# Optimization experiments

Measured on AMD Instinct MI355X. Metric: run time of the kernel, lower is better.

Reference implementation:

```python
import jax, jax.numpy as jnp
import numpy as np


def setup_inputs() -> dict:
    key = jax.random.key(0)
    k1, k2, k3 = jax.random.split(key, 3)
    B, C, H, W = 64, 512, 32, 32
    l = jax.random.normal(k1, (B, C, H, W), dtype=jnp.float32)
    g = jax.random.normal(k2, (B, C), dtype=jnp.float32)
    # 1x1 Conv2d(C -> 1, bias=False) weight, flattened from [1, C, 1, 1] to [C]
    w = jax.random.normal(k3, (C,), dtype=jnp.float32) * (1.0 / np.sqrt(C))
    return {"l": l, "g": g, "w": w}


def reference(l, g, w):
    B, C, H, W = l.shape
    # broadcast add of global vector, then 1x1 conv == channel dot-product
    x = l + g[:, :, None, None]                      # [B, C, H, W]
    c = jnp.einsum('bchw,c->bhw', x, w)              # [B, H, W]
    # softmax over the flattened spatial dims
    a = jax.nn.softmax(c.reshape(B, -1), axis=1).reshape(B, 1, H, W)
    # attention-weighted spatial pooling of l -> [B, C]
    g_out = jnp.einsum('bchw,bzhw->bc', l, a)
    return (c[:, None, :, :], g_out)
```

## Files before the change

### kernel.cpp

```cpp
#include <hip/hip_runtime.h>

#define B_  64
#define C_  512
#define HW_ 1024
#define NCHUNK 16
#define CPC (C_ / NCHUNK)

__device__ __forceinline__ float waveReduceSum(float v) {
    #pragma unroll
    for (int off = 32; off > 0; off >>= 1) v += __shfl_xor(v, off);
    return v;
}

__device__ __forceinline__ float waveReduceMax(float v) {
    #pragma unroll
    for (int off = 32; off > 0; off >>= 1) v = fmaxf(v, __shfl_xor(v, off));
    return v;
}

__global__ __launch_bounds__(256) void k1_partial_dot(
        const float* __restrict__ l,
        const float* __restrict__ w,
        float* __restrict__ part) {
    const int blk   = blockIdx.x;
    const int b     = blk / NCHUNK;
    const int chunk = blk % NCHUNK;
    const int tid   = threadIdx.x;

    const float4* l4 = reinterpret_cast<const float4*>(
        l + ((size_t)b * C_ + (size_t)chunk * CPC) * HW_);

    float4 acc = {0.f, 0.f, 0.f, 0.f};
    #pragma unroll 8
    for (int i = 0; i < CPC; ++i) {
        const float wv = w[chunk * CPC + i];
        const float4 v = l4[(size_t)i * (HW_ / 4) + tid];
        acc.x = fmaf(v.x, wv, acc.x);
        acc.y = fmaf(v.y, wv, acc.y);
        acc.z = fmaf(v.z, wv, acc.z);
        acc.w = fmaf(v.w, wv, acc.w);
    }
    reinterpret_cast<float4*>(part)[(size_t)blk * (HW_ / 4) + tid] = acc;
}

__global__ __launch_bounds__(1024) void k2_softmax(
        const float* __restrict__ part,
        const float* __restrict__ g,
        const float* __restrict__ w,
        float* __restrict__ c_out,
        float* __restrict__ a_out) {
    __shared__ float lds[16];
    const int b   = blockIdx.x;
    const int tid = threadIdx.x;
    const int lane = tid & 63;
    const int wid  = tid >> 6;

    float p = (tid < C_) ? g[b * C_ + tid] * w[tid] : 0.f;
    p = waveReduceSum(p);
    if (lane == 0) lds[wid] = p;
    __syncthreads();
    if (wid == 0) {
        float x = (lane < 16) ? lds[lane] : 0.f;
        x = waveReduceSum(x);
        if (lane == 0) lds[0] = x;
    }
    __syncthreads();
    const float gw = lds[0];
    __syncthreads();

    float cv = gw;
    #pragma unroll
    for (int k = 0; k < NCHUNK; ++k)
        cv += part[((size_t)b * NCHUNK + k) * HW_ + tid];

    float m = waveReduceMax(cv);
    if (lane == 0) lds[wid] = m;
    __syncthreads();
    if (wid == 0) {
        float x = (lane < 16) ? lds[lane] : -3.402823466e+38f;
        x = waveReduceMax(x);
        if (lane == 0) lds[0] = x;
    }
    __syncthreads();
    m = lds[0];
    __syncthreads();

    const float e = __expf(cv - m);
    float s = waveReduceSum(e);
    if (lane == 0) lds[wid] = s;
    __syncthreads();
    if (wid == 0) {
        float x = (lane < 16) ? lds[lane] : 0.f;
        x = waveReduceSum(x);
        if (lane == 0) lds[0] = x;
    }
    __syncthreads();
    s = lds[0];

    c_out[(size_t)b * HW_ + tid] = cv;
    a_out[(size_t)b * HW_ + tid] = e * __frcp_rn(s);
}

__global__ __launch_bounds__(256) void k3_pool(
        const float* __restrict__ l,
        const float* __restrict__ a,
        float* __restrict__ gout) {
    const int blk  = blockIdx.x;
    const int b    = blk >> 5;
    const int cg   = blk & 31;
    const int lane = threadIdx.x & 63;
    const int wave = threadIdx.x >> 6;

    const float4* a4 = reinterpret_cast<const float4*>(a + (size_t)b * HW_);
    float4 av[4];
    #pragma unroll
    for (int i = 0; i < 4; ++i) av[i] = a4[i * 64 + lane];

    #pragma unroll
    for (int ch = 0; ch < 4; ++ch) {
        const int c = cg * 16 + wave * 4 + ch;
        const float4* l4 = reinterpret_cast<const float4*>(
            l + ((size_t)b * C_ + c) * HW_);
        float s = 0.f;
        #pragma unroll
        for (int i = 0; i < 4; ++i) {
            const float4 v = l4[i * 64 + lane];
            s = fmaf(v.x, av[i].x, s);
            s = fmaf(v.y, av[i].y, s);
            s = fmaf(v.z, av[i].z, s);
            s = fmaf(v.w, av[i].w, s);
        }
        s = waveReduceSum(s);
        if (lane == 0) gout[(size_t)b * C_ + c] = s;
    }
}

extern "C" void kernel_launch(void* const* d_in, const int* in_sizes, int n_in,
                              void* d_out, int out_size, void* d_ws, size_t ws_size,
                              hipStream_t stream) {
    const float* l = (const float*)d_in[0];
    const float* g = (const float*)d_in[1];
    const float* w = (const float*)d_in[2];
    float* out = (float*)d_out;

    float* part = (float*)d_ws;
    float* a    = part + (size_t)B_ * NCHUNK * HW_;

    k1_partial_dot<<<B_ * NCHUNK, 256, 0, stream>>>(l, w, part);
    k2_softmax<<<B_, 1024, 0, stream>>>(part, g, w, out, a);
    k3_pool<<<B_ * 32, 256, 0, stream>>>(l, a, out + (size_t)B_ * HW_);
}
```

Measured before the change: 216.0 us.

## Fuse softmax into pooling kernel with per-block redundant softmax recompute

Merges the softmax kernel and the attention pooling kernel into one kernel launched with one block per (batch, channel chunk). Each block re-reduces the partial dot products, recomputes the softmax for its batch into shared memory, then pools its 32 channels. This removes a kernel launch, the low-occupancy 64-block softmax pass and the global round trip of the attention map. The cost is 16x redundant reads of the partial sums and redundant softmax work per batch.

New measurement: 217.6 us. No clear change (+0.7%).

```diff
diff --git a/kernel.cpp b/kernel.cpp
--- a/kernel.cpp
+++ b/kernel.cpp
@@ -18,7 +18,7 @@
     return v;
 }
 
-__global__ __launch_bounds__(256) void k1_partial_dot(
+__global__ __launch_bounds__(256) void kA_partial_dot(
         const float* __restrict__ l,
         const float* __restrict__ w,
         float* __restrict__ part) {
@@ -43,95 +43,84 @@
     reinterpret_cast<float4*>(part)[(size_t)blk * (HW_ / 4) + tid] = acc;
 }
 
-__global__ __launch_bounds__(1024) void k2_softmax(
+__global__ __launch_bounds__(256) void kB_softmax_pool(
+        const float* __restrict__ l,
         const float* __restrict__ part,
         const float* __restrict__ g,
         const float* __restrict__ w,
         float* __restrict__ c_out,
-        float* __restrict__ a_out) {
-    __shared__ float lds[16];
-    const int b   = blockIdx.x;
-    const int tid = threadIdx.x;
-    const int lane = tid & 63;
-    const int wid  = tid >> 6;
+        float* __restrict__ gout) {
+    __shared__ float a_lds[HW_];
+    __shared__ float red[4];
 
-    float p = (tid < C_) ? g[b * C_ + tid] * w[tid] : 0.f;
+    const int blk   = blockIdx.x;
+    const int b     = blk >> 4;
+    const int chunk = blk & 15;
+    const int tid   = threadIdx.x;
+    const int lane  = tid & 63;
+    const int wid   = tid >> 6;
+
+    float p = g[b * C_ + tid] * w[tid] + g[b * C_ + 256 + tid] * w[256 + tid];
     p = waveReduceSum(p);
-    if (lane == 0) lds[wid] = p;
+    if (lane == 0) red[wid] = p;
     __syncthreads();
-    if (wid == 0) {
-        float x = (lane < 16) ? lds[lane] : 0.f;
-        x = waveReduceSum(x);
-        if (lane == 0) lds[0] = x;
+    const float gw = red[0] + red[1] + red[2] + red[3];
+
+    const float4* part4 = reinterpret_cast<const float4*>(part);
+    float4 c4 = {gw, gw, gw, gw};
+    #pragma unroll
+    for (int k = 0; k < NCHUNK; ++k) {
+        const float4 v = part4[(size_t)(b * NCHUNK + k) * (HW_ / 4) + tid];
+        c4.x += v.x; c4.y += v.y; c4.z += v.z; c4.w += v.w;
     }
+
+    float m = fmaxf(fmaxf(c4.x, c4.y), fmaxf(c4.z, c4.w));
+    m = waveReduceMax(m);
     __syncthreads();
-    const float gw = lds[0];
+    if (lane == 0) red[wid] = m;
+    __syncthreads();
+    m = fmaxf(fmaxf(red[0], red[1]), fmaxf(red[2], red[3]));
+
+    float4 e4;
+    e4.x = __expf(c4.x - m);
+    e4.y = __expf(c4.y - m);
+    e4.z = __expf(c4.z - m);
+    e4.w = __expf(c4.w - m);
+    float s = e4.x + e4.y + e4.z + e4.w;
+    s = waveReduceSum(s);
+    __syncthreads();
+    if (lane == 0) red[wid] = s;
+    __syncthreads();
+    s = red[0] + red[1] + red[2] + red[3];
+    const float inv = __frcp_rn(s);
+
+    float4 a4 = {e4.x * inv, e4.y * inv, e4.z * inv, e4.w * inv};
+    reinterpret_cast<float4*>(a_lds)[tid] = a4;
+    if (chunk == 0)
+        reinterpret_cast<float4*>(c_out + (size_t)b * HW_)[tid] = c4;
     __syncthreads();
 
-    float cv = gw;
-    #pragma unroll
-    for (int k = 0; k < NCHUNK; ++k)
-        cv += part[((size_t)b * NCHUNK + k) * HW_ + tid];
-
-    float m = waveReduceMax(cv);
-    if (lane == 0) lds[wid] = m;
-    __syncthreads();
-    if (wid == 0) {
-        float x = (lane < 16) ? lds[lane] : -3.402823466e+38f;
-        x = waveReduceMax(x);
-        if (lane == 0) lds[0] = x;
-    }
-    __syncthreads();
-    m = lds[0];
-    __syncthreads();
-
-    const float e = __expf(cv - m);
-    float s = waveReduceSum(e);
-    if (lane == 0) lds[wid] = s;
-    __syncthreads();
-    if (wid == 0) {
-        float x = (lane < 16) ? lds[lane] : 0.f;
-        x = waveReduceSum(x);
-        if (lane == 0) lds[0] = x;
-    }
-    __syncthreads();
-    s = lds[0];
-
-    c_out[(size_t)b * HW_ + tid] = cv;
-    a_out[(size_t)b * HW_ + tid] = e * __frcp_rn(s);
-}
-
-__global__ __launch_bounds__(256) void k3_pool(
-        const float* __restrict__ l,
-        const float* __restrict__ a,
-        float* __restrict__ gout) {
-    const int blk  = blockIdx.x;
-    const int b    = blk >> 5;
-    const int cg   = blk & 31;
-    const int lane = threadIdx.x & 63;
-    const int wave = threadIdx.x >> 6;
-
-    const float4* a4 = reinterpret_cast<const float4*>(a + (size_t)b * HW_);
     float4 av[4];
     #pragma unroll
-    for (int i = 0; i < 4; ++i) av[i] = a4[i * 64 + lane];
+    for (int i = 0; i < 4; ++i)
+        av[i] = reinterpret_cast<float4*>(a_lds)[i * 64 + lane];
 
     #pragma unroll
-    for (int ch = 0; ch < 4; ++ch) {
-        const int c = cg * 16 + wave * 4 + ch;
+    for (int ch = 0; ch < 8; ++ch) {
+        const int c = chunk * CPC + wid * 8 + ch;
         const float4* l4 = reinterpret_cast<const float4*>(
             l + ((size_t)b * C_ + c) * HW_);
-        float s = 0.f;
+        float sacc = 0.f;
         #pragma unroll
         for (int i = 0; i < 4; ++i) {
             const float4 v = l4[i * 64 + lane];
-            s = fmaf(v.x, av[i].x, s);
-            s = fmaf(v.y, av[i].y, s);
-            s = fmaf(v.z, av[i].z, s);
-            s = fmaf(v.w, av[i].w, s);
+            sacc = fmaf(v.x, av[i].x, sacc);
+            sacc = fmaf(v.y, av[i].y, sacc);
+            sacc = fmaf(v.z, av[i].z, sacc);
+            sacc = fmaf(v.w, av[i].w, sacc);
         }
-        s = waveReduceSum(s);
-        if (lane == 0) gout[(size_t)b * C_ + c] = s;
+        sacc = waveReduceSum(sacc);
+        if (lane == 0) gout[(size_t)b * C_ + c] = sacc;
     }
 }
 
@@ -144,9 +133,8 @@
     float* out = (float*)d_out;
 
     float* part = (float*)d_ws;
-    float* a    = part + (size_t)B_ * NCHUNK * HW_;
 
-    k1_partial_dot<<<B_ * NCHUNK, 256, 0, stream>>>(l, w, part);
-    k2_softmax<<<B_, 1024, 0, stream>>>(part, g, w, out, a);
-    k3_pool<<<B_ * 32, 256, 0, stream>>>(l, a, out + (size_t)B_ * HW_);
+    kA_partial_dot<<<B_ * NCHUNK, 256, 0, stream>>>(l, w, part);
+    kB_softmax_pool<<<B_ * NCHUNK, 256, 0, stream>>>(
+        l, part, g, w, out, out + (size_t)B_ * HW_);
 }
```
